# Kernel tuning notes

Measured on AMD Instinct MI355X. Metric: run time of the kernel, lower is better.

The kernel has to match this reference:

```python
import jax, jax.numpy as jnp
import numpy as np

B, S, H, DH, D, FD, FU = 4, 256, 12, 64, 768, 2048, 2048


def setup_inputs() -> dict:
    key = jax.random.key(0)
    ks = jax.random.split(key, 12)
    s = 0.02  # typical init scale for weights
    return {
        "resid_pre": jax.random.normal(ks[0], (B, S, D), jnp.float32),
        "ln_scale": jax.random.uniform(ks[1], (B, S, 1), jnp.float32, 0.5, 2.0),
        "probs": jax.nn.softmax(jax.random.normal(ks[2], (B, H, S, S), jnp.float32), axis=-1),
        "W_O": jax.random.normal(ks[3], (H, DH, D), jnp.float32) * s,
        "W_V": jax.random.normal(ks[4], (H, D, DH), jnp.float32) * s,
        "enc_W": jax.random.normal(ks[5], (FD, D), jnp.float32) * s,
        "enc_b": jax.random.normal(ks[6], (FD,), jnp.float32) * s,
        "b_dec": jax.random.normal(ks[7], (D,), jnp.float32) * s,
        "up_dec_W": jax.random.normal(ks[8], (D, FU), jnp.float32) * s,
        "up_b_dec": jax.random.normal(ks[9], (D,), jnp.float32) * s,
        "pruned_features": jax.random.normal(ks[10], (B, S, FU), jnp.float32),
        "connection_mask": jax.random.randint(ks[11], (FD, FU), 0, 2, jnp.int32),
    }


def reference(resid_pre, ln_scale, probs, W_O, W_V, enc_W, enc_b, b_dec,
              up_dec_W, up_b_dec, pruned_features, connection_mask):
    # W_OV: [h, d_model(in), d_model(out)]
    W_OV = jnp.einsum('hko,hmk->hmo', W_O, W_V)
    mask = connection_mask.astype(resid_pre.dtype)

    # --- initial contributions ---
    act_ln = resid_pre / ln_scale                                  # [b,s,d]
    pre_moving = jnp.einsum('bsi,hio,fo->bshf', act_ln, W_OV, enc_W)  # [b,s,h,f_down]
    approx = jnp.einsum('bhqk,bkhf->bqf', probs, pre_moving)       # [b,q,f_down]

    # --- pruned contributions (one upstream AE) ---
    virtual = jnp.einsum('fo,hio,iu->hfu', enc_W, W_OV, up_dec_W) * mask[None]
    up_ln = pruned_features / ln_scale                             # [b,k,f_up]
    post_ov = jnp.einsum('bku,hfu->bhkf', up_ln, virtual)          # [b,h,k,f_down]
    approx = approx + jnp.einsum('bhqk,bhkf->bqf', probs, post_ov)

    # --- bias terms ---
    approx = approx + enc_b[None, None] - (enc_W @ b_dec)[None, None]
    ub_ln = up_b_dec[None, None] / ln_scale                        # [b,s,d]
    ub_post = jnp.einsum('hmd,bsm->bsd', W_OV, ub_ln)              # attn path through OV
    approx = approx + jnp.einsum('fd,bsd->bsf', enc_W, ub_post)
    return approx
```

## Files before the change

### kernel.cpp

```cpp
#include <hip/hip_runtime.h>
#include <hip/hip_bf16.h>
#include <stdint.h>

typedef __bf16 bf16;
typedef __bf16 bf16x8 __attribute__((ext_vector_type(8)));
typedef __bf16 bf16x4 __attribute__((ext_vector_type(4)));
typedef float f32x4 __attribute__((ext_vector_type(4)));

#define AS1 __attribute__((address_space(1)))
#define AS3 __attribute__((address_space(3)))


__device__ __forceinline__ void gld16(const bf16* g, bf16* l) {
  __builtin_amdgcn_global_load_lds((AS1 void*)g, (AS3 void*)l, 16, 0, 0);
}

__global__ void k_sentinel(float* __restrict__ out) {
  int i = blockIdx.x * 256 + threadIdx.x;
  if (i < 2097152) out[i] = 1048576.0f;
}

__global__ void k_prep(const float* __restrict__ lns, float* __restrict__ invln,
                       const float* __restrict__ enc_W, bf16* __restrict__ encWb,
                       const float* __restrict__ probs, bf16* __restrict__ probsT,
                       const int* __restrict__ cmask, bf16* __restrict__ maskb,
                       const float* __restrict__ W_O, bf16* __restrict__ WOb,
                       const float* __restrict__ resid, bf16* __restrict__ Xb,
                       bf16* __restrict__ BgTail, long ldTail) {
  const int bid = blockIdx.x, t = threadIdx.x;
  if (bid < 1) {
    for (int k = 0; k < 4; k++) { int j = t + k * 256; invln[j] = 1.0f / lns[j]; }
  } else if (bid < 1537) {
    long idx = ((long)(bid - 1) * 256 + t) * 4;
    float4 v = *(const float4*)(enc_W + idx);
    bf16x4 o; o[0]=(bf16)v.x; o[1]=(bf16)v.y; o[2]=(bf16)v.z; o[3]=(bf16)v.w;
    *(bf16x4*)(encWb + idx) = o;
  } else if (bid < 4609) {
    long idx = ((long)(bid - 1537) * 256 + t) * 4;
    int s = (int)(idx & 255), q = (int)((idx >> 8) & 255);
    int hb = (int)(idx >> 16), h = hb % 12, b = hb / 12;
    float4 v = *(const float4*)(probs + idx);
    bf16x4 o; o[0]=(bf16)v.x; o[1]=(bf16)v.y; o[2]=(bf16)v.z; o[3]=(bf16)v.w;
    *(bf16x4*)(probsT + (long)b * 786432 + (long)q * 3072 + h * 256 + s) = o;
  } else if (bid < 8705) {
    long idx = ((long)(bid - 4609) * 256 + t) * 4;
    int4 v = *(const int4*)(cmask + idx);
    bf16x4 o; o[0]=(bf16)(float)v.x; o[1]=(bf16)(float)v.y;
    o[2]=(bf16)(float)v.z; o[3]=(bf16)(float)v.w;
    *(bf16x4*)(maskb + idx) = o;
  } else if (bid < 9857) {
    long idx = ((long)(bid - 8705) * 256 + t) * 4;
    int o = (int)(idx % 768), r = (int)((idx / 768) & 127), h = (int)(idx / (768 * 128));
    bf16x4 ov;
    if (r < 64) {
      float4 v = *(const float4*)(W_O + (long)(h * 64 + r) * 768 + o);
      ov[0]=(bf16)v.x; ov[1]=(bf16)v.y; ov[2]=(bf16)v.z; ov[3]=(bf16)v.w;
    } else { ov[0]=ov[1]=ov[2]=ov[3]=(bf16)0.0f; }
    *(bf16x4*)(WOb + idx) = ov;
  } else if (bid < 10625) {
    long idx = ((long)(bid - 9857) * 256 + t) * 4;
    float il = 1.0f / lns[idx / 768];
    float4 v = *(const float4*)(resid + idx);
    bf16x4 o; o[0]=(bf16)(v.x*il); o[1]=(bf16)(v.y*il);
    o[2]=(bf16)(v.z*il); o[3]=(bf16)(v.w*il);
    *(bf16x4*)(Xb + idx) = o;
  } else {
    long idx = ((long)(bid - 10625) * 256 + t) * 4;
    int f = (int)(idx / 768), d = (int)(idx % 768);
    float4 v = *(const float4*)(enc_W + idx);
    bf16x4 o; o[0]=(bf16)v.x; o[1]=(bf16)v.y; o[2]=(bf16)v.z; o[3]=(bf16)v.w;
    *(bf16x4*)(BgTail + (long)f * ldTail + d) = o;
  }
}

__global__ void k_prepT(const float* __restrict__ wv, bf16* __restrict__ WVt,
                        const float* __restrict__ wo, bf16* __restrict__ W_Ot,
                        const float* __restrict__ updW, bf16* __restrict__ updWt,
                        const float* __restrict__ pr, const float* __restrict__ lns,
                        bf16* __restrict__ Ut) {
  __shared__ float tile[32][33];
  const int bid = blockIdx.x;
  int lane = threadIdx.x & 31, rg = threadIdx.x >> 5;
  if (bid < 1152) {
    int r0 = bid;
    int x = r0 % 4, y = (r0 / 4) % 24, h = r0 / 96;
    int k0 = x * 32, i0 = y * 32;
    if (k0 < 64) {
      for (int r = rg; r < 32; r += 8)
        tile[r][lane] = wv[((long)(h * 768 + i0 + r)) * 64 + k0 + lane];
      __syncthreads();
      for (int r = rg; r < 32; r += 8)
        WVt[((long)h * 128 + k0 + r) * 768 + i0 + lane] = (bf16)tile[lane][r];
    } else {
      for (int r = rg; r < 32; r += 8)
        WVt[((long)h * 128 + k0 + r) * 768 + i0 + lane] = (bf16)0.0f;
    }
  } else if (bid < 1728) {
    int r0 = bid - 1152;
    int x = r0 % 2, y = (r0 / 2) % 24, h = r0 / 48;
    int k0 = x * 32, o0 = y * 32;
    for (int r = rg; r < 32; r += 8)
      tile[r][lane] = wo[((long)(h * 64 + k0 + r)) * 768 + o0 + lane];
    __syncthreads();
    for (int r = rg; r < 32; r += 8)
      W_Ot[((long)(h * 768 + o0 + r)) * 64 + k0 + lane] = (bf16)tile[lane][r];
  } else if (bid < 3264) {
    int r0 = bid - 1728;
    int u0 = (r0 % 64) * 32, i0 = (r0 / 64) * 32;
    for (int r = rg; r < 32; r += 8)
      tile[r][lane] = updW[((long)(i0 + r)) * 2048 + u0 + lane];
    __syncthreads();
    for (int r = rg; r < 32; r += 8)
      updWt[((long)(u0 + r)) * 768 + i0 + lane] = (bf16)tile[lane][r];
  } else {
    int r0 = bid - 3264;
    int u0 = (r0 % 64) * 32, s0 = ((r0 / 64) % 8) * 32, b = r0 / 512;
    for (int r = rg; r < 32; r += 8) {
      int s = s0 + r;
      tile[r][lane] = pr[((long)(b * 256 + s)) * 2048 + u0 + lane] *
                      (1.0f / lns[b * 256 + s]);
    }
    __syncthreads();
    for (int r = rg; r < 32; r += 8)
      Ut[((long)b * 2048 + u0 + r) * 256 + s0 + lane] = (bf16)tile[lane][r];
  }
}

__global__ void k_sred(const float* __restrict__ Sp, bf16* __restrict__ dst, long ldd) {
  int i = blockIdx.x * 256 + threadIdx.x;
  if (i < 196608) {
    long idx = (long)i * 4;
    int m = (int)(idx / 768), o = (int)(idx % 768);
    float4 v = *(const float4*)(Sp + idx);
    float4 a = *(const float4*)(Sp + 786432 + idx);
    float4 b = *(const float4*)(Sp + 2 * 786432 + idx);
    float4 c = *(const float4*)(Sp + 3 * 786432 + idx);
    v.x += a.x + b.x + c.x; v.y += a.y + b.y + c.y;
    v.z += a.z + b.z + c.z; v.w += a.w + b.w + c.w;
    bf16x4 ov;
    ov[0] = (bf16)v.x; ov[1] = (bf16)v.y; ov[2] = (bf16)v.z; ov[3] = (bf16)v.w;
    *(bf16x4*)(dst + (long)m * ldd + o) = ov;
  }
}


__device__ __forceinline__ float blk_reduce(float s) {
  __shared__ float red[256];
  red[threadIdx.x] = s; __syncthreads();
  for (int o = 128; o > 0; o >>= 1) {
    if ((int)threadIdx.x < o) red[threadIdx.x] += red[threadIdx.x + o];
    __syncthreads();
  }
  float r = red[0]; __syncthreads();
  return r;
}

__global__ void k_bias_t(const float* __restrict__ W_V, const float* __restrict__ up_b,
                         float* __restrict__ t_hk) {
  int j = blockIdx.x, h = j >> 6, k = j & 63;
  float s = 0.f;
  for (int m = threadIdx.x; m < 768; m += 256)
    s += W_V[((long)(h * 768 + m)) * 64 + k] * up_b[m];
  float r = blk_reduce(s);
  if (threadIdx.x == 0) t_hk[j] = r;
}

__global__ void k_bias_w(const float* __restrict__ W_O, const float* __restrict__ t_hk,
                         float* __restrict__ w) {
  int d = blockIdx.x;
  float s = 0.f;
  for (int j = threadIdx.x; j < 768; j += 256)
    s += W_O[(long)j * 768 + d] * t_hk[j];
  float r = blk_reduce(s);
  if (threadIdx.x == 0) w[d] = r;
}

__global__ void k_bias_c(const float* __restrict__ enc_W, const float* __restrict__ enc_b,
                         const float* __restrict__ b_dec, const float* __restrict__ w,
                         float* __restrict__ c0, float* __restrict__ c1) {
  int f = blockIdx.x;
  float s0 = 0.f, s1 = 0.f;
  for (int d = threadIdx.x; d < 768; d += 256) {
    float e = enc_W[(long)f * 768 + d];
    s0 += e * b_dec[d];
    s1 += e * w[d];
  }
  float r0 = blk_reduce(s0);
  float r1 = blk_reduce(s1);
  if (threadIdx.x == 0) { c0[f] = enc_b[f] - r0; c1[f] = r1; }
}

__global__ __launch_bounds__(256)
void gemm_bt(const bf16* __restrict__ A, const bf16* __restrict__ B, void* __restrict__ Cv,
             int M, int N, int K,
             long lda, long ldb, long ldc,
             int batchH,
             long sa_b, long sa_h, long sb_b, long sb_h, long sc_b, long sc_h,
             int mode, int kChunk,
             const bf16* __restrict__ mask, long mask_ld)
{
  __shared__ __align__(16) bf16 Asm[128 * 64];
  __shared__ __align__(16) bf16 Bsm[128 * 64];

  const int t = threadIdx.x;

  const int nbx = gridDim.x, nby = gridDim.y;
  const int nxy = nbx * nby;
  int orig = blockIdx.x + nbx * blockIdx.y;
  int qq = nxy >> 3, rr = nxy & 7;
  int xcd = orig & 7, lid = orig >> 3;
  int swz = (xcd < rr) ? (xcd * (qq + 1) + lid)
                       : (rr * (qq + 1) + (xcd - rr) * qq + lid);
  const int m0 = (swz % nby) * 128;
  const int n0 = (swz / nby) * 128;

  long aoff, boff, coff;
  int k0, k1;
  if (mode == 4) {
    int z = blockIdx.z;
    int bb = z / batchH, kc = z - bb * batchH;
    aoff = (long)bb * sa_b;
    boff = (long)bb * sb_b;
    coff = (long)bb * sc_b + (long)kc * sc_h;
    k0 = kc * kChunk; k1 = k0 + kChunk; if (k1 > K) k1 = K;
  } else if (mode >= 2) {
    int z = blockIdx.z;
    aoff = 0; boff = 0;
    coff = (long)z * (long)M * ldc;
    k0 = z * kChunk; k1 = k0 + kChunk; if (k1 > K) k1 = K;
  } else {
    int z = blockIdx.z;
    int bb = z / batchH, hh = z - bb * batchH;
    aoff = (long)bb * sa_b + (long)hh * sa_h;
    boff = (long)bb * sb_b + (long)hh * sb_h;
    coff = (long)bb * sc_b + (long)hh * sc_h;
    k0 = 0; k1 = K;
  }

  const bf16* Ab = A + aoff + (long)m0 * lda;
  const bf16* Bb = B + boff + (long)n0 * ldb;

  const int r0 = t >> 3;
  const int g8 = t & 7;

  const int L = t & 63, w = t >> 6;
  const int wm = (w & 1) * 64, wn = (w >> 1) * 64;
  const int r16 = L & 15, q = L >> 4;

  f32x4 acc[4][4];
#pragma unroll
  for (int i = 0; i < 4; i++)
#pragma unroll
    for (int j = 0; j < 4; j++) acc[i][j] = (f32x4){0.f, 0.f, 0.f, 0.f};

  for (int kt = k0; kt < k1; kt += 64) {
#pragma unroll
    for (int j = 0; j < 4; j++) {
      int row = j * 32 + r0;
      int sc = ((g8 ^ (row & 7)) << 3);
      gld16(Ab + (long)row * lda + (kt + sc), &Asm[j * 2048 + t * 8]);
      gld16(Bb + (long)row * ldb + (kt + sc), &Bsm[j * 2048 + t * 8]);
    }
    __syncthreads();

#pragma unroll
    for (int h2 = 0; h2 < 2; h2++) {
      bf16x8 af[4], bfr[4];
#pragma unroll
      for (int i = 0; i < 4; i++) {
        int ra = wm + i * 16 + r16;
        af[i]  = *(const bf16x8*)&Asm[ra * 64 + ((((h2 << 2) + q) ^ (ra & 7)) << 3)];
        int rb = wn + i * 16 + r16;
        bfr[i] = *(const bf16x8*)&Bsm[rb * 64 + ((((h2 << 2) + q) ^ (rb & 7)) << 3)];
      }
#pragma unroll
      for (int mi = 0; mi < 4; mi++)
#pragma unroll
        for (int ni = 0; ni < 4; ni++)
          acc[mi][ni] = __builtin_amdgcn_mfma_f32_16x16x32_bf16(af[mi], bfr[ni], acc[mi][ni], 0, 0, 0);
    }
    __syncthreads();
  }

  if (mode >= 2) {
    float* C = (float*)Cv;
#pragma unroll
    for (int mi = 0; mi < 4; mi++)
#pragma unroll
      for (int ni = 0; ni < 4; ni++)
#pragma unroll
        for (int r = 0; r < 4; r++) {
          int gm = m0 + wm + mi * 16 + q * 4 + r;
          int gn = n0 + wn + ni * 16 + r16;
          long idx = coff + (long)gm * ldc + gn;
          float v = acc[mi][ni][r];
          if (mode == 3) v += C[idx];
          C[idx] = v;
        }
  } else {
    bf16* C = (bf16*)Cv;
#pragma unroll
    for (int mi = 0; mi < 4; mi++)
#pragma unroll
      for (int ni = 0; ni < 4; ni++)
#pragma unroll
        for (int r = 0; r < 4; r++) {
          int gm = m0 + wm + mi * 16 + q * 4 + r;
          int gn = n0 + wn + ni * 16 + r16;
          float v = acc[mi][ni][r];
          if (mode == 1) v *= (float)mask[(long)gm * mask_ld + gn];
          C[coff + (long)gm * ldc + gn] = (bf16)v;
        }
  }
}

__global__ __launch_bounds__(512, 4)
void gemm_fp3(const bf16* __restrict__ A, const bf16* __restrict__ B,
              float* __restrict__ C,
              int M, int N, int K, long lda, long ldb, long ldc,
              int mode, int kChunk)
{
  __shared__ __align__(16) bf16 SM[2][12288];

  const int t = threadIdx.x;

  const int nz = gridDim.z;
  int fid = blockIdx.x + gridDim.x * (blockIdx.y + gridDim.y * blockIdx.z);
  const int z  = fid % nz;
  const int t2 = fid / nz;
  const int m0 = (t2 & 7) * 128;
  const int n0 = (t2 >> 3) * 256;

  const long coff = (long)z * (long)M * ldc;
  int k0 = z * kChunk, k1 = k0 + kChunk; if (k1 > K) k1 = K;
  const int NT = (k1 > k0) ? (k1 - k0) >> 5 : 0;

  const bf16* Ab = A + (long)m0 * lda + k0;
  const bf16* Bb = B + (long)n0 * ldb + k0;

  const int L = t & 63, w = t >> 6;
  const int wm = (w & 1) * 64;
  const int wn = (w >> 1) * 64;
  const int r16 = L & 15, q = L >> 4;

  f32x4 acc[4][4];
#pragma unroll
  for (int i = 0; i < 4; i++)
#pragma unroll
    for (int j = 0; j < 4; j++) acc[i][j] = (f32x4){0.f, 0.f, 0.f, 0.f};

  auto stage = [&](int tt, int buf) {
    const bf16* Ap = Ab + (long)tt * 32;
    const bf16* Bp = Bb + (long)tt * 32;
    {
      int row = t >> 2, g2 = t & 3;
      gld16(Ap + (long)row * lda + ((g2 ^ ((row >> 1) & 3)) << 3), &SM[buf][t * 8]);
    }
#pragma unroll
    for (int j = 0; j < 2; j++) {
      int slot = j * 512 + t;
      int row = slot >> 2, g2 = slot & 3;
      gld16(Bp + (long)row * ldb + ((g2 ^ ((row >> 1) & 3)) << 3),
            &SM[buf][4096 + slot * 8]);
    }
  };

  if (NT >= 1) stage(0, 0);

  for (int tt = 0; tt < NT; tt++) {
    if (tt + 1 < NT) {
      stage(tt + 1, (tt + 1) & 1);
      asm volatile("s_waitcnt vmcnt(3)" ::: "memory");
    } else {
      asm volatile("s_waitcnt vmcnt(0)" ::: "memory");
    }
    __builtin_amdgcn_s_barrier();

    const bf16* As = &SM[tt & 1][0];
    const bf16* Bs = &SM[tt & 1][4096];
    bf16x8 af[4], bfr[4];
#pragma unroll
    for (int i = 0; i < 4; i++) {
      int ra = wm + i * 16 + r16;
      af[i]  = *(const bf16x8*)&As[ra * 32 + ((q ^ ((ra >> 1) & 3)) << 3)];
    }
#pragma unroll
    for (int i = 0; i < 4; i++) {
      int rb = wn + i * 16 + r16;
      bfr[i] = *(const bf16x8*)&Bs[rb * 32 + ((q ^ ((rb >> 1) & 3)) << 3)];
    }
#pragma unroll
    for (int mi = 0; mi < 4; mi++)
#pragma unroll
      for (int ni = 0; ni < 4; ni++)
        acc[mi][ni] = __builtin_amdgcn_mfma_f32_16x16x32_bf16(af[mi], bfr[ni], acc[mi][ni], 0, 0, 0);
    __builtin_amdgcn_s_barrier();
  }

#pragma unroll
  for (int mi = 0; mi < 4; mi++)
#pragma unroll
    for (int ni = 0; ni < 4; ni++)
#pragma unroll
      for (int r = 0; r < 4; r++) {
        int gm = m0 + wm + mi * 16 + q * 4 + r;
        int gn = n0 + wn + ni * 16 + r16;
        long idx = coff + (long)gm * ldc + gn;
        float v = acc[mi][ni][r];
        if (mode == 3) v += C[idx];
        C[idx] = v;
      }
}

__global__ void k_out(const float* __restrict__ Cp, const float* __restrict__ c0,
                      const float* __restrict__ c1, const float* __restrict__ invln,
                      float* __restrict__ out, int nsplit) {
  int i4 = blockIdx.x * 256 + threadIdx.x;
  long i = (long)i4 * 4;
  int n = (int)(i & 2047), m = (int)(i >> 11);
  float4 v = *(const float4*)(Cp + i);
  for (int z = 1; z < nsplit; z++) {
    float4 u = *(const float4*)(Cp + i + (long)z * 2097152);
    v.x += u.x; v.y += u.y; v.z += u.z; v.w += u.w;
  }
  float il = invln[m];
  float4 a = *(const float4*)(c0 + n);
  float4 b = *(const float4*)(c1 + n);
  v.x += a.x + b.x * il;
  v.y += a.y + b.y * il;
  v.z += a.z + b.z * il;
  v.w += a.w + b.w * il;
  *(float4*)(out + i) = v;
}


extern "C" void kernel_launch(void* const* d_in, const int* in_sizes, int n_in,
                              void* d_out, int out_size, void* d_ws, size_t ws_size,
                              hipStream_t stream) {
  (void)out_size;
  float* out = (float*)d_out;

  int iresid = -1, iln = -1, iprobs = -1, iencb = -1, ipruned = -1, imask = -1;
  int iwo = -1, iwv = -1, iencw = -1, iupdw = -1, ibdec = -1, iupb = -1;
  for (int i = 0; i < n_in; i++) {
    switch (in_sizes[i]) {
      case 786432:  iresid  = i; break;
      case 1024:    iln     = i; break;
      case 3145728: iprobs  = i; break;
      case 2048:    iencb   = i; break;
      case 2097152: ipruned = i; break;
      case 4194304: imask   = i; break;
      case 589824:  if (iwo   < 0) iwo   = i; else iwv   = i; break;
      case 1572864: if (iencw < 0) iencw = i; else iupdw = i; break;
      case 768:     if (ibdec < 0) ibdec = i; else iupb  = i; break;
      default: break;
    }
  }
  bool ok = n_in == 12 && iresid >= 0 && iln >= 0 && iprobs >= 0 && iencb >= 0 &&
            ipruned >= 0 && imask >= 0 && iwo >= 0 && iwv >= 0 && iencw >= 0 &&
            iupdw >= 0 && ibdec >= 0 && iupb >= 0;
  if (!ok) { k_sentinel<<<8192, 256, 0, stream>>>(out); return; }

  const float* resid = (const float*)d_in[iresid];
  const float* lns   = (const float*)d_in[iln];
  const float* probs = (const float*)d_in[iprobs];
  const float* W_O   = (const float*)d_in[iwo];
  const float* W_V   = (const float*)d_in[iwv];
  const float* enc_W = (const float*)d_in[iencw];
  const float* enc_b = (const float*)d_in[iencb];
  const float* b_dec = (const float*)d_in[ibdec];
  const float* updW  = (const float*)d_in[iupdw];
  const float* up_b  = (const float*)d_in[iupb];
  const float* pruned= (const float*)d_in[ipruned];
  const int*   cmask = (const int*)d_in[imask];

  auto pad = [](size_t b) -> size_t { return (b + 255) & ~(size_t)255; };
  const size_t prepB = pad(2359296) + pad(2359296) + pad(3145728) + pad(1572864) +
                       pad(3145728) + pad(1179648) + pad(3145728) + pad(18874368) +
                       pad(12582912);
  const size_t persB = pad(6291456) + pad(4194304) + pad(6291456) + pad(6291456) +
                       pad(8388608) + pad(4096) + pad(3072) + pad(3072) +
                       pad(8192) + pad(8192);
  auto needB = [&](int g, int ns) -> size_t {
    size_t cp = (size_t)ns * 8388608;
    size_t ov = prepB > cp ? prepB : cp;
    long KA = (long)g * 2048 + 768;
    size_t ab = pad((size_t)1024 * KA * 2) + pad((size_t)2048 * KA * 2);
    return ov + persB + ab + (2ull << 20);
  };
  const int cgs[14] = {12, 12, 12, 6, 6, 4, 3, 2, 2, 1, 1, 1, 1, 1};
  const int cns[14] = { 8,  4, 2, 8, 4, 4, 4, 4, 2, 8, 4, 2, 2, 1};
  int gs = 0, nsplit = 0;
  for (int ci = 0; ci < 14; ci++) {
    if (needB(cgs[ci], cns[ci]) <= ws_size) { gs = cgs[ci]; nsplit = cns[ci]; break; }
  }
  if (gs == 0) { gs = 1; nsplit = 1; }

  const long KA = (long)gs * 2048 + 768;

  char* p = (char*)d_ws;
  auto alloc = [&](size_t bytes) -> char* {
    char* r = p; p += (bytes + 255) & ~(size_t)255; return r;
  };
  char* overlayBase = p;
  bf16*  WOb    = (bf16*)alloc(12ull * 128 * 768 * 2);
  bf16*  WVt    = (bf16*)alloc(12ull * 128 * 768 * 2);
  bf16*  updWt  = (bf16*)alloc(2048ull * 768 * 2);
  bf16*  Xb     = (bf16*)alloc(1024ull * 768 * 2);
  bf16*  encWb  = (bf16*)alloc(2048ull * 768 * 2);
  bf16*  W_Ot   = (bf16*)alloc(12ull * 768 * 64 * 2);
  bf16*  T1     = (bf16*)alloc(12ull * 1024 * 128 * 2);
  bf16*  T3     = (bf16*)alloc(4ull * 768 * 3072 * 2);
  float* Sp     = (float*)alloc(4ull * 1024 * 768 * 4);
  {
    size_t used = (size_t)(p - overlayBase);
    size_t cp = (size_t)nsplit * 8388608;
    p = overlayBase + (used > cp ? used : cp);
  }
  float* Cpart  = (float*)overlayBase;
  bf16*  G_t    = (bf16*)alloc(12ull * 2048 * 128 * 2);
  bf16*  Ut     = (bf16*)alloc(4ull * 2048 * 256 * 2);
  bf16*  E1     = (bf16*)alloc(12ull * 2048 * 128 * 2);
  bf16*  probsT = (bf16*)alloc(4ull * 256 * 3072 * 2);
  bf16*  maskb  = (bf16*)alloc(2048ull * 2048 * 2);
  float* invln  = (float*)alloc(1024 * 4);
  float* t_hk   = (float*)alloc(768 * 4);
  float* wv     = (float*)alloc(768 * 4);
  float* c0     = (float*)alloc(2048 * 4);
  float* c1     = (float*)alloc(2048 * 4);
  bf16*  A_g    = (bf16*)alloc((size_t)1024 * KA * 2);
  bf16*  B_g    = (bf16*)alloc((size_t)2048 * KA * 2);

  k_prep<<<12161, 256, 0, stream>>>(lns, invln, enc_W, encWb, probs, probsT,
                                    cmask, maskb, W_O, WOb, resid, Xb,
                                    B_g + (long)gs * 2048, KA);
  k_prepT<<<5312, 256, 0, stream>>>(W_V, WVt, W_O, W_Ot, updW, updWt,
                                    pruned, lns, Ut);
  k_bias_t<<<768, 256, 0, stream>>>(W_V, up_b, t_hk);
  k_bias_w<<<768, 256, 0, stream>>>(W_O, t_hk, wv);
  k_bias_c<<<2048, 256, 0, stream>>>(enc_W, enc_b, b_dec, wv, c0, c1);

  gemm_bt<<<dim3(1, 16, 24), 256, 0, stream>>>(
      encWb, WOb, E1, 2048, 128, 768,
      768, 768, 128, 12,
      (long)(updWt - encWb), 0,
      (long)(WVt - WOb), (long)128 * 768,
      (long)(G_t - E1), (long)2048 * 128,
      0, 0, nullptr, 0);

  gemm_bt<<<dim3(1, 8, 12), 256, 0, stream>>>(
      Xb, WVt, T1, 1024, 128, 768,
      768, 768, 128, 12,
      0, 0, 0, (long)128 * 768, 0, (long)1024 * 128,
      0, 0, nullptr, 0);

  gemm_bt<<<dim3(2, 6, 48), 256, 0, stream>>>(
      W_Ot, T1, T3, 768, 256, 64,
      64, 128, 3072, 12,
      0, (long)768 * 64, (long)256 * 128, (long)1024 * 128, 2359296, 256,
      0, 0, nullptr, 0);

  gemm_bt<<<dim3(6, 2, 16), 256, 0, stream>>>(
      probsT, T3, Sp, 256, 768, 3072,
      3072, 3072, 768, 4,
      786432, 0, 2359296, 0, 196608, 786432,
      4, 768, nullptr, 0);

  k_sred<<<768, 256, 0, stream>>>(Sp, A_g + (long)gs * 2048, KA);

  for (int g = 0; g < 12 / gs; g++) {
    gemm_bt<<<dim3(16, 16, gs), 256, 0, stream>>>(
        E1 + (long)g * gs * 2048 * 128, G_t + (long)g * gs * 2048 * 128, B_g,
        2048, 2048, 64,
        128, 128, KA, gs,
        0, (long)2048 * 128, 0, (long)2048 * 128, 0, 2048,
        1, 0, maskb, 2048);

    gemm_bt<<<dim3(16, 2, 4 * gs), 256, 0, stream>>>(
        probsT + (long)g * gs * 256, Ut, A_g,
        256, 2048, 256,
        3072, 256, KA, gs,
        786432, 256, (long)2048 * 256, 0, 256 * KA, 2048,
        0, 0, nullptr, 0);

    int Kthis = (g == 0) ? (int)KA : gs * 2048;
    int kc = ((Kthis / nsplit + 63) / 64) * 64;
    gemm_fp3<<<dim3(8, 8, nsplit), 512, 0, stream>>>(
        A_g, B_g, Cpart,
        1024, 2048, Kthis,
        KA, KA, 2048,
        (g == 0) ? 2 : 3, kc);
  }

  k_out<<<2048, 256, 0, stream>>>(Cpart, c0, c1, invln, out, nsplit);
}
```

Measured before the change: 444.5 us.

## Enlarge final GEMM tile to 256x256 with direct-to-register B loads

The final split-K GEMM moves from 128x256 tiles with K-step 32 to 256x256 tiles with K-step 64. Only A is staged through LDS, with a wider XOR swizzle. B fragments are loaded straight from global memory into registers and double-buffered with ping-pong register sets. The aim is fewer blocks, more MFMA work per LDS read and less LDS traffic for B, in exchange for much higher register pressure (launch bounds drop to 2), half as many blocks, and uncoalesced per-lane B loads.

New measurement: 481.2 us. 8.3% more time.

```diff
diff --git a/kernel.cpp b/kernel.cpp
--- a/kernel.cpp
+++ b/kernel.cpp
@@ -314,13 +314,13 @@
   }
 }
 
-__global__ __launch_bounds__(512, 4)
-void gemm_fp3(const bf16* __restrict__ A, const bf16* __restrict__ B,
+__global__ __launch_bounds__(512, 2)
+void gemm_fp4(const bf16* __restrict__ A, const bf16* __restrict__ B,
               float* __restrict__ C,
               int M, int N, int K, long lda, long ldb, long ldc,
               int mode, int kChunk)
 {
-  __shared__ __align__(16) bf16 SM[2][12288];
+  __shared__ __align__(16) bf16 SM[2][16384];
 
   const int t = threadIdx.x;
 
@@ -328,77 +328,119 @@
   int fid = blockIdx.x + gridDim.x * (blockIdx.y + gridDim.y * blockIdx.z);
   const int z  = fid % nz;
   const int t2 = fid / nz;
-  const int m0 = (t2 & 7) * 128;
-  const int n0 = (t2 >> 3) * 256;
+  const int m0 = (t2 >> 3) * 256;
+  const int n0 = (t2 & 7) * 256;
 
   const long coff = (long)z * (long)M * ldc;
   int k0 = z * kChunk, k1 = k0 + kChunk; if (k1 > K) k1 = K;
-  const int NT = (k1 > k0) ? (k1 - k0) >> 5 : 0;
+  const int NT = (k1 > k0) ? (k1 - k0) >> 6 : 0;
 
   const bf16* Ab = A + (long)m0 * lda + k0;
-  const bf16* Bb = B + (long)n0 * ldb + k0;
+
+  const int sr = t >> 3;
+  const int g8 = t & 7;
 
   const int L = t & 63, w = t >> 6;
-  const int wm = (w & 1) * 64;
+  const int wm = (w & 1) * 128;
   const int wn = (w >> 1) * 64;
   const int r16 = L & 15, q = L >> 4;
 
-  f32x4 acc[4][4];
-#pragma unroll
-  for (int i = 0; i < 4; i++)
+  const bf16* Bp0 = B + (long)(n0 + wn + 0 * 16 + r16) * ldb + k0 + q * 8;
+  const bf16* Bp1 = B + (long)(n0 + wn + 1 * 16 + r16) * ldb + k0 + q * 8;
+  const bf16* Bp2 = B + (long)(n0 + wn + 2 * 16 + r16) * ldb + k0 + q * 8;
+  const bf16* Bp3 = B + (long)(n0 + wn + 3 * 16 + r16) * ldb + k0 + q * 8;
+
+  f32x4 acc[8][4];
+#pragma unroll
+  for (int i = 0; i < 8; i++)
 #pragma unroll
     for (int j = 0; j < 4; j++) acc[i][j] = (f32x4){0.f, 0.f, 0.f, 0.f};
 
-  auto stage = [&](int tt, int buf) {
-    const bf16* Ap = Ab + (long)tt * 32;
-    const bf16* Bp = Bb + (long)tt * 32;
+  auto stageA = [&](int tt, int buf) {
+    const bf16* Ap = Ab + (long)tt * 64;
+#pragma unroll
+    for (int j = 0; j < 4; j++) {
+      int row = j * 64 + sr;
+      int sc = ((g8 ^ (row & 7)) << 3);
+      gld16(Ap + (long)row * lda + sc, &SM[buf][j * 4096 + t * 8]);
+    }
+  };
+
+  bf16x8 b0[2][4], b1[2][4];
+
+#define LOADB(DST, tt) do {                                         \
+    long kk_ = (long)(tt) * 64;                                     \
+    DST[0][0] = *(const bf16x8*)(Bp0 + kk_);                        \
+    DST[0][1] = *(const bf16x8*)(Bp1 + kk_);                        \
+    DST[0][2] = *(const bf16x8*)(Bp2 + kk_);                        \
+    DST[0][3] = *(const bf16x8*)(Bp3 + kk_);                        \
+    DST[1][0] = *(const bf16x8*)(Bp0 + kk_ + 32);                   \
+    DST[1][1] = *(const bf16x8*)(Bp1 + kk_ + 32);                   \
+    DST[1][2] = *(const bf16x8*)(Bp2 + kk_ + 32);                   \
+    DST[1][3] = *(const bf16x8*)(Bp3 + kk_ + 32);                   \
+  } while (0)
+
+#define COMPUTE(BC, ASRC) do {                                      \
+    _Pragma("unroll")                                               \
+    for (int h2 = 0; h2 < 2; h2++) {                                \
+      bf16x8 af[8];                                                 \
+      _Pragma("unroll")                                             \
+      for (int i = 0; i < 8; i++) {                                 \
+        int ra = wm + i * 16 + r16;                                 \
+        af[i] = *(const bf16x8*)&(ASRC)[ra * 64 +                   \
+                 ((((h2 << 2) + q) ^ (ra & 7)) << 3)];              \
+      }                                                             \
+      _Pragma("unroll")                                             \
+      for (int mi = 0; mi < 8; mi++)                                \
+        _Pragma("unroll")                                           \
+        for (int ni = 0; ni < 4; ni++)                              \
+          acc[mi][ni] = __builtin_amdgcn_mfma_f32_16x16x32_bf16(    \
+              af[mi], (BC)[h2][ni], acc[mi][ni], 0, 0, 0);          \
+    }                                                               \
+  } while (0)
+
+  if (NT >= 1) { stageA(0, 0); LOADB(b0, 0); }
+
+  int tt = 0;
+  while (tt < NT) {
     {
-      int row = t >> 2, g2 = t & 3;
-      gld16(Ap + (long)row * lda + ((g2 ^ ((row >> 1) & 3)) << 3), &SM[buf][t * 8]);
-    }
-#pragma unroll
-    for (int j = 0; j < 2; j++) {
-      int slot = j * 512 + t;
-      int row = slot >> 2, g2 = slot & 3;
-      gld16(Bp + (long)row * ldb + ((g2 ^ ((row >> 1) & 3)) << 3),
-            &SM[buf][4096 + slot * 8]);
-    }
-  };
-
-  if (NT >= 1) stage(0, 0);
-
-  for (int tt = 0; tt < NT; tt++) {
-    if (tt + 1 < NT) {
-      stage(tt + 1, (tt + 1) & 1);
-      asm volatile("s_waitcnt vmcnt(3)" ::: "memory");
-    } else {
-      asm volatile("s_waitcnt vmcnt(0)" ::: "memory");
-    }
-    __builtin_amdgcn_s_barrier();
-
-    const bf16* As = &SM[tt & 1][0];
-    const bf16* Bs = &SM[tt & 1][4096];
-    bf16x8 af[4], bfr[4];
-#pragma unroll
-    for (int i = 0; i < 4; i++) {
-      int ra = wm + i * 16 + r16;
-      af[i]  = *(const bf16x8*)&As[ra * 32 + ((q ^ ((ra >> 1) & 3)) << 3)];
-    }
-#pragma unroll
-    for (int i = 0; i < 4; i++) {
-      int rb = wn + i * 16 + r16;
-      bfr[i] = *(const bf16x8*)&Bs[rb * 32 + ((q ^ ((rb >> 1) & 3)) << 3)];
-    }
-#pragma unroll
-    for (int mi = 0; mi < 4; mi++)
-#pragma unroll
-      for (int ni = 0; ni < 4; ni++)
-        acc[mi][ni] = __builtin_amdgcn_mfma_f32_16x16x32_bf16(af[mi], bfr[ni], acc[mi][ni], 0, 0, 0);
-    __builtin_amdgcn_s_barrier();
-  }
-
-#pragma unroll
-  for (int mi = 0; mi < 4; mi++)
+      bool more = (tt + 1 < NT);
+      if (more) {
+        stageA(tt + 1, (tt + 1) & 1);
+        LOADB(b1, tt + 1);
+        asm volatile("s_waitcnt vmcnt(12)" ::: "memory");
+      } else {
+        asm volatile("s_waitcnt vmcnt(0)" ::: "memory");
+      }
+      __builtin_amdgcn_s_barrier();
+      const bf16* As = &SM[tt & 1][0];
+      COMPUTE(b0, As);
+      __builtin_amdgcn_s_barrier();
+      tt++;
+      if (!more) break;
+    }
+    {
+      bool more = (tt + 1 < NT);
+      if (more) {
+        stageA(tt + 1, (tt + 1) & 1);
+        LOADB(b0, tt + 1);
+        asm volatile("s_waitcnt vmcnt(12)" ::: "memory");
+      } else {
+        asm volatile("s_waitcnt vmcnt(0)" ::: "memory");
+      }
+      __builtin_amdgcn_s_barrier();
+      const bf16* As = &SM[tt & 1][0];
+      COMPUTE(b1, As);
+      __builtin_amdgcn_s_barrier();
+      tt++;
+      if (!more) break;
+    }
+  }
+#undef LOADB
+#undef COMPUTE
+
+#pragma unroll
+  for (int mi = 0; mi < 8; mi++)
 #pragma unroll
     for (int ni = 0; ni < 4; ni++)
 #pragma unroll
@@ -585,7 +627,7 @@
 
     int Kthis = (g == 0) ? (int)KA : gs * 2048;
     int kc = ((Kthis / nsplit + 63) / 64) * 64;
-    gemm_fp3<<<dim3(8, 8, nsplit), 512, 0, stream>>>(
+    gemm_fp4<<<dim3(8, 4, nsplit), 512, 0, stream>>>(
         A_g, B_g, Cpart,
         1024, 2048, Kthis,
         KA, KA, 2048,
```

## Enlarge final split-K GEMM tile to 256x256 with BK=64 and interleaved MFMA

Applied to the files above, without the earlier changes.

Replaces the 128x256 tile, BK=32 split-K GEMM with a 256x256 tile and BK=64. Each wave now holds a 128x64 accumulator, and LDS uses a wider XOR swizzle. Fragment loads are interleaved between MFMA groups using sched_barrier and setprio, so LDS reads overlap matrix math. The aim is more reuse per byte loaded and fewer barriers per K step, at the cost of more registers and LDS (occupancy drops from 4 to 2 blocks) and half as many blocks in the grid.

Result: no change. 436.5 us (-1.8%).

```diff
diff --git a/kernel.cpp b/kernel.cpp
--- a/kernel.cpp
+++ b/kernel.cpp
@@ -314,13 +314,13 @@
   }
 }
 
-__global__ __launch_bounds__(512, 4)
-void gemm_fp3(const bf16* __restrict__ A, const bf16* __restrict__ B,
+__global__ __launch_bounds__(512, 2)
+void gemm_fp2(const bf16* __restrict__ A, const bf16* __restrict__ B,
               float* __restrict__ C,
               int M, int N, int K, long lda, long ldb, long ldc,
               int mode, int kChunk)
 {
-  __shared__ __align__(16) bf16 SM[2][12288];
+  __shared__ __align__(16) bf16 SM[2][2][16384];
 
   const int t = threadIdx.x;
 
@@ -328,40 +328,44 @@
   int fid = blockIdx.x + gridDim.x * (blockIdx.y + gridDim.y * blockIdx.z);
   const int z  = fid % nz;
   const int t2 = fid / nz;
-  const int m0 = (t2 & 7) * 128;
-  const int n0 = (t2 >> 3) * 256;
+  const int m0 = (t2 >> 3) * 256;
+  const int n0 = (t2 & 7) * 256;
 
   const long coff = (long)z * (long)M * ldc;
   int k0 = z * kChunk, k1 = k0 + kChunk; if (k1 > K) k1 = K;
-  const int NT = (k1 > k0) ? (k1 - k0) >> 5 : 0;
+  const int NT = (k1 > k0) ? (k1 - k0) >> 6 : 0;
 
   const bf16* Ab = A + (long)m0 * lda + k0;
   const bf16* Bb = B + (long)n0 * ldb + k0;
 
+  const int sr = t >> 3;
+  const int g8 = t & 7;
+
   const int L = t & 63, w = t >> 6;
-  const int wm = (w & 1) * 64;
+  const int wm = (w & 1) * 128;
   const int wn = (w >> 1) * 64;
   const int r16 = L & 15, q = L >> 4;
 
-  f32x4 acc[4][4];
-#pragma unroll
-  for (int i = 0; i < 4; i++)
+  f32x4 acc[8][4];
+#pragma unroll
+  for (int i = 0; i < 8; i++)
 #pragma unroll
     for (int j = 0; j < 4; j++) acc[i][j] = (f32x4){0.f, 0.f, 0.f, 0.f};
 
   auto stage = [&](int tt, int buf) {
-    const bf16* Ap = Ab + (long)tt * 32;
-    const bf16* Bp = Bb + (long)tt * 32;
-    {
-      int row = t >> 2, g2 = t & 3;
-      gld16(Ap + (long)row * lda + ((g2 ^ ((row >> 1) & 3)) << 3), &SM[buf][t * 8]);
-    }
-#pragma unroll
-    for (int j = 0; j < 2; j++) {
-      int slot = j * 512 + t;
-      int row = slot >> 2, g2 = slot & 3;
-      gld16(Bp + (long)row * ldb + ((g2 ^ ((row >> 1) & 3)) << 3),
-            &SM[buf][4096 + slot * 8]);
+    const bf16* Ap = Ab + (long)tt * 64;
+    const bf16* Bp = Bb + (long)tt * 64;
+#pragma unroll
+    for (int j = 0; j < 4; j++) {
+      int row = j * 64 + sr;
+      int sc = ((g8 ^ (row & 7)) << 3);
+      gld16(Ap + (long)row * lda + sc, &SM[buf][0][j * 4096 + t * 8]);
+    }
+#pragma unroll
+    for (int j = 0; j < 4; j++) {
+      int row = j * 64 + sr;
+      int sc = ((g8 ^ (row & 7)) << 3);
+      gld16(Bp + (long)row * ldb + sc, &SM[buf][1][j * 4096 + t * 8]);
     }
   };
 
@@ -370,35 +374,84 @@
   for (int tt = 0; tt < NT; tt++) {
     if (tt + 1 < NT) {
       stage(tt + 1, (tt + 1) & 1);
-      asm volatile("s_waitcnt vmcnt(3)" ::: "memory");
+      asm volatile("s_waitcnt vmcnt(8)" ::: "memory");
     } else {
       asm volatile("s_waitcnt vmcnt(0)" ::: "memory");
     }
     __builtin_amdgcn_s_barrier();
 
-    const bf16* As = &SM[tt & 1][0];
-    const bf16* Bs = &SM[tt & 1][4096];
-    bf16x8 af[4], bfr[4];
+    const bf16* As = &SM[tt & 1][0][0];
+    const bf16* Bs = &SM[tt & 1][1][0];
+
+    bf16x8 a0[4], a1[4], bq0[4], bq1[4];
 #pragma unroll
     for (int i = 0; i < 4; i++) {
       int ra = wm + i * 16 + r16;
-      af[i]  = *(const bf16x8*)&As[ra * 32 + ((q ^ ((ra >> 1) & 3)) << 3)];
+      a0[i] = *(const bf16x8*)&As[ra * 64 + ((q ^ (ra & 7)) << 3)];
     }
 #pragma unroll
     for (int i = 0; i < 4; i++) {
       int rb = wn + i * 16 + r16;
-      bfr[i] = *(const bf16x8*)&Bs[rb * 32 + ((q ^ ((rb >> 1) & 3)) << 3)];
-    }
+      bq0[i] = *(const bf16x8*)&Bs[rb * 64 + ((q ^ (rb & 7)) << 3)];
+    }
+#pragma unroll
+    for (int i = 0; i < 4; i++) {
+      int ra = wm + (4 + i) * 16 + r16;
+      a1[i] = *(const bf16x8*)&As[ra * 64 + ((q ^ (ra & 7)) << 3)];
+    }
+    __builtin_amdgcn_sched_barrier(0);
+    __builtin_amdgcn_s_setprio(1);
 #pragma unroll
     for (int mi = 0; mi < 4; mi++)
 #pragma unroll
       for (int ni = 0; ni < 4; ni++)
-        acc[mi][ni] = __builtin_amdgcn_mfma_f32_16x16x32_bf16(af[mi], bfr[ni], acc[mi][ni], 0, 0, 0);
+        acc[mi][ni] = __builtin_amdgcn_mfma_f32_16x16x32_bf16(a0[mi], bq0[ni], acc[mi][ni], 0, 0, 0);
+    __builtin_amdgcn_s_setprio(0);
+#pragma unroll
+    for (int i = 0; i < 4; i++) {
+      int ra = wm + i * 16 + r16;
+      a0[i] = *(const bf16x8*)&As[ra * 64 + (((4 + q) ^ (ra & 7)) << 3)];
+    }
+#pragma unroll
+    for (int i = 0; i < 4; i++) {
+      int rb = wn + i * 16 + r16;
+      bq1[i] = *(const bf16x8*)&Bs[rb * 64 + (((4 + q) ^ (rb & 7)) << 3)];
+    }
+    __builtin_amdgcn_sched_barrier(0);
+    __builtin_amdgcn_s_setprio(1);
+#pragma unroll
+    for (int mi = 0; mi < 4; mi++)
+#pragma unroll
+      for (int ni = 0; ni < 4; ni++)
+        acc[4 + mi][ni] = __builtin_amdgcn_mfma_f32_16x16x32_bf16(a1[mi], bq0[ni], acc[4 + mi][ni], 0, 0, 0);
+    __builtin_amdgcn_s_setprio(0);
+#pragma unroll
+    for (int i = 0; i < 4; i++) {
+      int ra = wm + (4 + i) * 16 + r16;
+      a1[i] = *(const bf16x8*)&As[ra * 64 + (((4 + q) ^ (ra & 7)) << 3)];
+    }
+    __builtin_amdgcn_sched_barrier(0);
+    __builtin_amdgcn_s_setprio(1);
+#pragma unroll
+    for (int mi = 0; mi < 4; mi++)
+#pragma unroll
+      for (int ni = 0; ni < 4; ni++)
+        acc[mi][ni] = __builtin_amdgcn_mfma_f32_16x16x32_bf16(a0[mi], bq1[ni], acc[mi][ni], 0, 0, 0);
+    __builtin_amdgcn_s_setprio(0);
+    __builtin_amdgcn_sched_barrier(0);
+    __builtin_amdgcn_s_setprio(1);
+#pragma unroll
+    for (int mi = 0; mi < 4; mi++)
+#pragma unroll
+      for (int ni = 0; ni < 4; ni++)
+        acc[4 + mi][ni] = __builtin_amdgcn_mfma_f32_16x16x32_bf16(a1[mi], bq1[ni], acc[4 + mi][ni], 0, 0, 0);
+    __builtin_amdgcn_s_setprio(0);
+
     __builtin_amdgcn_s_barrier();
   }
 
 #pragma unroll
-  for (int mi = 0; mi < 4; mi++)
+  for (int mi = 0; mi < 8; mi++)
 #pragma unroll
     for (int ni = 0; ni < 4; ni++)
 #pragma unroll
@@ -585,7 +638,7 @@
 
     int Kthis = (g == 0) ? (int)KA : gs * 2048;
     int kc = ((Kthis / nsplit + 63) / 64) * 64;
-    gemm_fp3<<<dim3(8, 8, nsplit), 512, 0, stream>>>(
+    gemm_fp2<<<dim3(8, 4, nsplit), 512, 0, stream>>>(
         A_g, B_g, Cpart,
         1024, 2048, Kthis,
         KA, KA, 2048,
```
